# Kernel tuning notes

Measured on AMD Instinct MI355X. Metric: run time of the kernel, lower is better.

Reference implementation:

```python
import jax, jax.numpy as jnp
import numpy as np

B, S, E, H = 2, 2048, 1024, 16
D = E // H


def setup_inputs() -> dict:
    key = jax.random.key(0)
    ks = jax.random.split(key, 11)
    def lin(k):
        kw, kb = jax.random.split(k)
        bound = 1.0 / np.sqrt(E)
        W = jax.random.uniform(kw, (E, E), jnp.float32, -bound, bound)
        b = jax.random.uniform(kb, (E,), jnp.float32, -bound, bound)
        return W, b
    Wq, bq = lin(ks[0])
    Wk, bk = lin(ks[1])
    Wv, bv = lin(ks[2])
    Wo, bo = lin(ks[3])
    return {
        "query": jax.random.normal(ks[4], (B, S, E), jnp.float32),
        "key": jax.random.normal(ks[5], (B, S, E), jnp.float32),
        "value": jax.random.normal(ks[6], (B, S, E), jnp.float32),
        "Wq": Wq, "bq": bq, "Wk": Wk, "bk": bk,
        "Wv": Wv, "bv": bv, "Wo": Wo, "bo": bo,
        "is_causal": 1,
    }


def reference(query, key, value, Wq, bq, Wk, bk, Wv, bv, Wo, bo, is_causal):
    scale = D ** -0.5
    def heads(x, W, b):
        # torch Linear: x @ W.T + b, then [B,S,H,D] -> [B,H,S,D]
        y = jnp.einsum('bse,fe->bsf', x, W) + b
        return y.reshape(B, S, H, D).transpose(0, 2, 1, 3)
    q = heads(query, Wq, bq)
    k = heads(key, Wk, bk)
    v = heads(value, Wv, bv)
    scores = jnp.einsum('bhqd,bhkd->bhqk', q, k) * scale  # [B,H,S,S]
    if is_causal:
        mask = jnp.tril(jnp.ones((S, S), dtype=bool))
        scores = jnp.where(mask, scores, -jnp.inf)
    attn = jax.nn.softmax(scores, axis=-1)
    out = jnp.einsum('bhqk,bhkd->bhqd', attn, v)
    out = out.transpose(0, 2, 1, 3).reshape(B, S, E)
    return jnp.einsum('bse,fe->bsf', out, Wo) + bo
```

## Files before the change

kernel.cpp:

```cpp
#include <hip/hip_runtime.h>
#include <cstdint>
#include <cstddef>

typedef unsigned short u16;
typedef unsigned int u32;
typedef __attribute__((ext_vector_type(8))) short bf16x8;
typedef __attribute__((ext_vector_type(4))) float f32x4;
typedef __attribute__((ext_vector_type(16))) float f32x16;
typedef __attribute__((ext_vector_type(4))) u16 u16x4;
typedef __attribute__((ext_vector_type(4))) u32 u32x4;
typedef __attribute__((ext_vector_type(2))) u32 u32x2;

__device__ __forceinline__ u16 f2bf(float f) {
  u32 x = __builtin_bit_cast(u32, f);
  x += 0x7fffu + ((x >> 16) & 1u);
  return (u16)(x >> 16);
}

__device__ __forceinline__ void g2lds16(const u16* g, u16* l) {
  __builtin_amdgcn_global_load_lds(
      (const __attribute__((address_space(1))) u32*)g,
      (__attribute__((address_space(3))) u32*)l, 16, 0, 0);
}

struct CvtArgs { const float* s[7]; u16* d[7]; int n4[7]; };

__global__ __launch_bounds__(256) void cvt_all(CvtArgs a) {
  int y = blockIdx.y;
  const float4* __restrict__ src = (const float4*)a.s[y];
  u16* __restrict__ dst = a.d[y];
  int n4 = a.n4[y];
  for (int i = blockIdx.x * blockDim.x + threadIdx.x; i < n4;
       i += gridDim.x * blockDim.x) {
    float4 v = src[i];
    u16x4 o = { f2bf(v.x), f2bf(v.y), f2bf(v.z), f2bf(v.w) };
    *(u16x4*)(dst + (size_t)i * 4) = o;
  }
}

struct GemmArgs {
  const u16* A[3]; const u16* W[3]; const float* bias[3];
  void* out[3]; float scale[3]; int mode[3];
};

__global__ __launch_bounds__(256) void gemm_fused(GemmArgs ga) {
  __shared__ alignas(16) u16 As[2][128 * 32];
  __shared__ alignas(16) u16 Bs[2][128 * 32];
  const int z = blockIdx.z;
  const u16* __restrict__ A = ga.A[z];
  const u16* __restrict__ W = ga.W[z];
  const int tid = threadIdx.x;
  const int lane = tid & 63;
  const int w = tid >> 6;
  const int lo4 = lane & 15, hi2 = lane >> 4;
  const int l = (int)blockIdx.x + 8 * (int)blockIdx.y;
  const int wl = (l & 7) * 32 + (l >> 3);
  const int m0 = (wl >> 3) * 128;
  const int n0 = (wl & 7) * 128;
  const int wr = w >> 1, wc = w & 1;

  f32x4 acc[4][4] = {};

  auto stage = [&](int kt, int buf) {
    const int k0 = kt * 32;
#pragma unroll
    for (int i = 0; i < 2; ++i) {
      int c = (i * 4 + w) * 64 + lane;
      int r = c >> 2;
      int q = (c & 3) ^ ((r >> 1) & 3);
      g2lds16(A + (size_t)(m0 + r) * 1024 + k0 + q * 8, As[buf] + (i * 4 + w) * 512);
      g2lds16(W + (size_t)(n0 + r) * 1024 + k0 + q * 8, Bs[buf] + (i * 4 + w) * 512);
    }
  };

  stage(0, 0);
  __syncthreads();
  int cur = 0;
  for (int kt = 0; kt < 32; ++kt) {
    if (kt + 1 < 32) stage(kt + 1, cur ^ 1);
    bf16x8 af[4], bfr[4];
#pragma unroll
    for (int i = 0; i < 4; ++i) {
      int r = wr * 64 + i * 16 + lo4;
      int q = hi2 ^ ((r >> 1) & 3);
      af[i] = *(const bf16x8*)(As[cur] + r * 32 + q * 8);
    }
#pragma unroll
    for (int j = 0; j < 4; ++j) {
      int r = wc * 64 + j * 16 + lo4;
      int q = hi2 ^ ((r >> 1) & 3);
      bfr[j] = *(const bf16x8*)(Bs[cur] + r * 32 + q * 8);
    }
#pragma unroll
    for (int i = 0; i < 4; ++i)
#pragma unroll
      for (int j = 0; j < 4; ++j)
        acc[i][j] = __builtin_amdgcn_mfma_f32_16x16x32_bf16(af[i], bfr[j], acc[i][j], 0, 0, 0);
    __syncthreads();
    cur ^= 1;
  }

  const float* __restrict__ bias = ga.bias[z];
  const float cs = ga.scale[z];
  const int mode = ga.mode[z];
#pragma unroll
  for (int j = 0; j < 4; ++j) {
    int n = n0 + wc * 64 + j * 16 + lo4;
    float bv = bias[n];
#pragma unroll
    for (int i = 0; i < 4; ++i) {
#pragma unroll
      for (int rg = 0; rg < 4; ++rg) {
        int m = m0 + wr * 64 + i * 16 + hi2 * 4 + rg;
        float v = (acc[i][j][rg] + bv) * cs;
        if (mode == 2) {
          ((float*)ga.out[z])[(size_t)m * 1024 + n] = v;
        } else {
          int b = m >> 11, s = m & 2047, h = n >> 6, d = n & 63;
          size_t addr = (mode == 0)
            ? ((size_t)(b * 16 + h) * 2048 + s) * 64 + d
            : ((size_t)(b * 16 + h) * 64 + d) * 2048 + s;
          ((u16*)ga.out[z])[addr] = f2bf(v);
        }
      }
    }
  }
}

__global__ __launch_bounds__(256, 2) void attn_kernel(
    const u16* __restrict__ Q, const u16* __restrict__ K,
    const u16* __restrict__ Vt, u16* __restrict__ Out,
    const int* __restrict__ causal_p) {
  __shared__ alignas(16) u16 Ks[2][2][64 * 64];
  __shared__ alignas(16) u16 Vs[2][2][64 * 64];
  const int tid = threadIdx.x, lane = tid & 63, w = tid >> 6;
  const int wg = w >> 1, wv = w & 1;
  const int ql = lane & 31, hi = lane >> 5;
  const int bh = blockIdx.y;
  const int qt = (bh < 16) ? (int)blockIdx.x : 15 - (int)blockIdx.x;
  const int causal = *causal_p;
  const u16* Qb = Q + (size_t)bh * 2048 * 64;
  const u16* Kb = K + (size_t)bh * 2048 * 64;
  const u16* Vb = Vt + (size_t)bh * 64 * 2048;

  const int qA = qt * 128 + wv * 64 + ql;
  const int qB = qA + 32;

  bf16x8 qfA[4], qfB[4];
#pragma unroll
  for (int dsl = 0; dsl < 4; ++dsl) {
    qfA[dsl] = *(const bf16x8*)(Qb + (size_t)qA * 64 + dsl * 16 + hi * 8);
    qfB[dsl] = *(const bf16x8*)(Qb + (size_t)qB * 64 + dsl * 16 + hi * 8);
  }

  auto stageKV = [&](int jt, int buf) {
#pragma unroll
    for (int i = 0; i < 4; ++i) {
      int c = i * 128 + wv * 64 + lane;
      int r = c >> 3;
      int q = (c & 7) ^ (r & 7);
      g2lds16(Kb + (size_t)(jt * 64 + r) * 64 + q * 8, Ks[wg][buf] + (i * 128 + wv * 64) * 8);
      g2lds16(Vb + (size_t)r * 2048 + jt * 64 + q * 8, Vs[wg][buf] + (i * 128 + wv * 64) * 8);
    }
  };

  const int nt_w = causal ? (2 * qt + wv + 1) : 32;
  const int U = causal ? (qt + 1) : 16;

  stageKV(wg, 0);
  __syncthreads();

  float mA = -1e30f, lA = 0.f, mB = -1e30f, lB = 0.f;
  f32x16 oA0 = {}, oA1 = {}, oB0 = {}, oB1 = {};
  int cur = 0;

  auto online_sm = [&](f32x16& s0, f32x16& s1, float& m_r, float& l_r,
                       f32x16& o0, f32x16& o1) {
    float pm = fmaxf(s0[0], s1[0]);
#pragma unroll
    for (int rg = 1; rg < 16; ++rg) pm = fmaxf(pm, fmaxf(s0[rg], s1[rg]));
    pm = fmaxf(pm, __shfl_xor(pm, 32));
    if (!__all(pm <= m_r + 8.f)) {
      float mn = fmaxf(m_r, pm);
      float corr = exp2f(m_r - mn);
      m_r = mn; l_r *= corr;
#pragma unroll
      for (int rg = 0; rg < 16; ++rg) { o0[rg] *= corr; o1[rg] *= corr; }
    }
    float sum = 0.f;
#pragma unroll
    for (int rg = 0; rg < 16; ++rg) { s0[rg] = exp2f(s0[rg] - m_r); sum += s0[rg]; }
#pragma unroll
    for (int rg = 0; rg < 16; ++rg) { s1[rg] = exp2f(s1[rg] - m_r); sum += s1[rg]; }
    sum += __shfl_xor(sum, 32);
    l_r += sum;
  };

  for (int u = 0; u < U; ++u) {
    const int jt = 2 * u + wg;
    if (u + 1 < U) stageKV(jt + 2, cur ^ 1);

    if (jt < nt_w) {
      f32x16 sA0 = {}, sA1 = {}, sB0 = {}, sB1 = {};
#pragma unroll
      for (int dsl = 0; dsl < 4; ++dsl) {
        int cc = dsl * 2 + hi;
        bf16x8 k0 = *(const bf16x8*)(Ks[wg][cur] + ql * 64 + ((cc ^ (ql & 7)) * 8));
        bf16x8 k1 = *(const bf16x8*)(Ks[wg][cur] + (32 + ql) * 64 + ((cc ^ (ql & 7)) * 8));
        sA0 = __builtin_amdgcn_mfma_f32_32x32x16_bf16(k0, qfA[dsl], sA0, 0, 0, 0);
        sB0 = __builtin_amdgcn_mfma_f32_32x32x16_bf16(k0, qfB[dsl], sB0, 0, 0, 0);
        sA1 = __builtin_amdgcn_mfma_f32_32x32x16_bf16(k1, qfA[dsl], sA1, 0, 0, 0);
        sB1 = __builtin_amdgcn_mfma_f32_32x32x16_bf16(k1, qfB[dsl], sB1, 0, 0, 0);
      }

      if (causal && jt == nt_w - 1) {
#pragma unroll
        for (int rg = 0; rg < 16; ++rg) {
          int kof = jt * 64 + 8 * (rg >> 2) + (rg & 3) + 4 * hi;
          sA0[rg] = (kof > qA) ? -1e30f : sA0[rg];
          sA1[rg] = (kof + 32 > qA) ? -1e30f : sA1[rg];
          sB0[rg] = (kof > qB) ? -1e30f : sB0[rg];
          sB1[rg] = (kof + 32 > qB) ? -1e30f : sB1[rg];
        }
      }

      online_sm(sA0, sA1, mA, lA, oA0, oA1);
      online_sm(sB0, sB1, mB, lB, oB0, oB1);

#pragma unroll
      for (int s = 0; s < 4; ++s) {
        const f32x16& pA = (s >= 2) ? sA1 : sA0;
        const f32x16& pB = (s >= 2) ? sB1 : sB0;
        const int base = 8 * (s & 1);
        u32 a0, a1, b0, b1, c0, c1, d0_, d1;
        asm("v_cvt_pk_bf16_f32 %0, %1, %2" : "=v"(a0) : "v"(pA[base + 0]), "v"(pA[base + 1]));
        asm("v_cvt_pk_bf16_f32 %0, %1, %2" : "=v"(a1) : "v"(pA[base + 2]), "v"(pA[base + 3]));
        asm("v_cvt_pk_bf16_f32 %0, %1, %2" : "=v"(b0) : "v"(pA[base + 4]), "v"(pA[base + 5]));
        asm("v_cvt_pk_bf16_f32 %0, %1, %2" : "=v"(b1) : "v"(pA[base + 6]), "v"(pA[base + 7]));
        asm volatile("v_permlane32_swap_b32 %0, %1" : "+v"(a0), "+v"(b0));
        asm volatile("v_permlane32_swap_b32 %0, %1" : "+v"(a1), "+v"(b1));
        asm("v_cvt_pk_bf16_f32 %0, %1, %2" : "=v"(c0) : "v"(pB[base + 0]), "v"(pB[base + 1]));
        asm("v_cvt_pk_bf16_f32 %0, %1, %2" : "=v"(c1) : "v"(pB[base + 2]), "v"(pB[base + 3]));
        asm("v_cvt_pk_bf16_f32 %0, %1, %2" : "=v"(d0_) : "v"(pB[base + 4]), "v"(pB[base + 5]));
        asm("v_cvt_pk_bf16_f32 %0, %1, %2" : "=v"(d1) : "v"(pB[base + 6]), "v"(pB[base + 7]));
        asm volatile("v_permlane32_swap_b32 %0, %1" : "+v"(c0), "+v"(d0_));
        asm volatile("v_permlane32_swap_b32 %0, %1" : "+v"(c1), "+v"(d1));
        u32x4 pwA = {a0, a1, b0, b1};
        u32x4 pwB = {c0, c1, d0_, d1};
        bf16x8 pfA = __builtin_bit_cast(bf16x8, pwA);
        bf16x8 pfB = __builtin_bit_cast(bf16x8, pwB);
#pragma unroll
        for (int df = 0; df < 2; ++df) {
          int rr = df * 32 + ql;
          bf16x8 vf = *(const bf16x8*)(Vs[wg][cur] + rr * 64 + (((s * 2 + hi) ^ (rr & 7)) * 8));
          if (df) {
            oA1 = __builtin_amdgcn_mfma_f32_32x32x16_bf16(vf, pfA, oA1, 0, 0, 0);
            oB1 = __builtin_amdgcn_mfma_f32_32x32x16_bf16(vf, pfB, oB1, 0, 0, 0);
          } else {
            oA0 = __builtin_amdgcn_mfma_f32_32x32x16_bf16(vf, pfA, oA0, 0, 0, 0);
            oB0 = __builtin_amdgcn_mfma_f32_32x32x16_bf16(vf, pfB, oB0, 0, 0, 0);
          }
        }
      }
    }
    __syncthreads();
    cur ^= 1;
  }

  float* Od = (float*)&Ks[0][0][0];
  float* ml = (float*)&Vs[0][0][0];
  const int li = wv * 64 + lane;
  if (wg == 1) {
#pragma unroll
    for (int rg = 0; rg < 16; ++rg) {
      Od[((li * 2 + 0) * 2 + 0) * 16 + rg] = oA0[rg];
      Od[((li * 2 + 0) * 2 + 1) * 16 + rg] = oA1[rg];
      Od[((li * 2 + 1) * 2 + 0) * 16 + rg] = oB0[rg];
      Od[((li * 2 + 1) * 2 + 1) * 16 + rg] = oB1[rg];
    }
    ml[li * 4 + 0] = mA; ml[li * 4 + 1] = lA;
    ml[li * 4 + 2] = mB; ml[li * 4 + 3] = lB;
  }
  __syncthreads();
  if (wg == 0) {
    const int batch = bh >> 4, h = bh & 15;
#pragma unroll
    for (int sub = 0; sub < 2; ++sub) {
      float m_r = sub ? mB : mA;
      float l_r = sub ? lB : lA;
      float m_b = ml[li * 4 + sub * 2 + 0];
      float l_b = ml[li * 4 + sub * 2 + 1];
      float mn = fmaxf(m_r, m_b);
      float ca = exp2f(m_r - mn), cb = exp2f(m_b - mn);
      float rl = 1.f / (l_r * ca + l_b * cb);
      int qrow = sub ? qB : qA;
      u16* orow = Out + ((size_t)(batch * 2048 + qrow)) * 1024 + h * 64;
#pragma unroll
      for (int df = 0; df < 2; ++df) {
        const f32x16& oo = sub ? (df ? oB1 : oB0) : (df ? oA1 : oA0);
        const float* Op = &Od[((li * 2 + sub) * 2 + df) * 16];
#pragma unroll
        for (int b2 = 0; b2 < 4; ++b2) {
          u32 w0, w1;
          float v0 = (oo[4 * b2 + 0] * ca + Op[4 * b2 + 0] * cb) * rl;
          float v1 = (oo[4 * b2 + 1] * ca + Op[4 * b2 + 1] * cb) * rl;
          float v2 = (oo[4 * b2 + 2] * ca + Op[4 * b2 + 2] * cb) * rl;
          float v3 = (oo[4 * b2 + 3] * ca + Op[4 * b2 + 3] * cb) * rl;
          asm("v_cvt_pk_bf16_f32 %0, %1, %2" : "=v"(w0) : "v"(v0), "v"(v1));
          asm("v_cvt_pk_bf16_f32 %0, %1, %2" : "=v"(w1) : "v"(v2), "v"(v3));
          int d0 = df * 32 + b2 * 8 + hi * 4;
          u32x2 pr = {w0, w1};
          *(u32x2*)(orow + d0) = pr;
        }
      }
    }
  }
}

extern "C" void kernel_launch(void* const* d_in, const int* in_sizes, int n_in,
                              void* d_out, int out_size, void* d_ws, size_t ws_size,
                              hipStream_t stream) {
  (void)in_sizes; (void)n_in; (void)out_size; (void)ws_size;
  const float* query = (const float*)d_in[0];
  const float* key   = (const float*)d_in[1];
  const float* value = (const float*)d_in[2];
  const float* Wq = (const float*)d_in[3];
  const float* bq = (const float*)d_in[4];
  const float* Wk = (const float*)d_in[5];
  const float* bk = (const float*)d_in[6];
  const float* Wv = (const float*)d_in[7];
  const float* bv = (const float*)d_in[8];
  const float* Wo = (const float*)d_in[9];
  const float* bo = (const float*)d_in[10];
  const int* is_causal = (const int*)d_in[11];

  u16* wsp = (u16*)d_ws;
  u16* xq  = wsp;
  u16* xk  = xq  + (4u << 20);
  u16* xv  = xk  + (4u << 20);
  u16* wq  = xv  + (4u << 20);
  u16* wk  = wq  + (1u << 20);
  u16* wv  = wk  + (1u << 20);
  u16* wo  = wv  + (1u << 20);
  u16* Qb  = wo  + (1u << 20);
  u16* Kb  = Qb  + (4u << 20);
  u16* Vtb = Kb  + (4u << 20);
  u16* attn= Vtb + (4u << 20);

  CvtArgs ca;
  ca.s[0] = query; ca.d[0] = xq; ca.n4[0] = 1 << 20;
  ca.s[1] = key;   ca.d[1] = xk; ca.n4[1] = 1 << 20;
  ca.s[2] = value; ca.d[2] = xv; ca.n4[2] = 1 << 20;
  ca.s[3] = Wq; ca.d[3] = wq; ca.n4[3] = 1 << 18;
  ca.s[4] = Wk; ca.d[4] = wk; ca.n4[4] = 1 << 18;
  ca.s[5] = Wv; ca.d[5] = wv; ca.n4[5] = 1 << 18;
  ca.s[6] = Wo; ca.d[6] = wo; ca.n4[6] = 1 << 18;
  cvt_all<<<dim3(512, 7), 256, 0, stream>>>(ca);

  const float LOG2E = 1.4426950408889634f;
  GemmArgs g1;
  g1.A[0] = xq; g1.W[0] = wq; g1.bias[0] = bq; g1.out[0] = Qb;
  g1.scale[0] = 0.125f * LOG2E; g1.mode[0] = 0;
  g1.A[1] = xk; g1.W[1] = wk; g1.bias[1] = bk; g1.out[1] = Kb;
  g1.scale[1] = 1.f; g1.mode[1] = 0;
  g1.A[2] = xv; g1.W[2] = wv; g1.bias[2] = bv; g1.out[2] = Vtb;
  g1.scale[2] = 1.f; g1.mode[2] = 1;
  gemm_fused<<<dim3(8, 32, 3), 256, 0, stream>>>(g1);

  attn_kernel<<<dim3(16, 32), 256, 0, stream>>>(Qb, Kb, Vtb, attn, is_causal);

  GemmArgs g2;
  for (int i = 0; i < 3; ++i) {
    g2.A[i] = attn; g2.W[i] = wo; g2.bias[i] = bo; g2.out[i] = d_out;
    g2.scale[i] = 1.f; g2.mode[i] = 2;
  }
  gemm_fused<<<dim3(8, 32, 1), 256, 0, stream>>>(g2);
}
```

Measured before the change: 142.9 us.

## Replace GEMM with 256x256-tile 8-wave kernel using interleaved staging and MFMA priority

The projection GEMMs move from 128x128 tiles with 4 waves and K=32 steps to 256x256 tiles with 8 waves and K=64 steps. Global-to-LDS staging of the next k-tile is interleaved between four MFMA quadrants, with explicit vmcnt waits, barriers and setprio around the MFMA bursts. This is meant to raise arithmetic intensity and overlap memory with compute. The grid shrinks to 64 blocks per GEMM (192 for QKV), which may underfill the GPU, and the 128 KB of LDS per block limits occupancy.

New measurement: 170.2 us. 19.1% more time.

```diff
diff --git a/kernel.cpp b/kernel.cpp
--- a/kernel.cpp
+++ b/kernel.cpp
@@ -43,76 +43,123 @@
   void* out[3]; float scale[3]; int mode[3];
 };
 
-__global__ __launch_bounds__(256) void gemm_fused(GemmArgs ga) {
-  __shared__ alignas(16) u16 As[2][128 * 32];
-  __shared__ alignas(16) u16 Bs[2][128 * 32];
+__global__ __launch_bounds__(512, 2) void gemm8(GemmArgs ga) {
+  __shared__ alignas(16) u16 As[2][2][128 * 64];
+  __shared__ alignas(16) u16 Bs[2][2][128 * 64];
   const int z = blockIdx.z;
   const u16* __restrict__ A = ga.A[z];
   const u16* __restrict__ W = ga.W[z];
-  const int tid = threadIdx.x;
-  const int lane = tid & 63;
-  const int w = tid >> 6;
+  const int tid = threadIdx.x, lane = tid & 63, w = tid >> 6;
   const int lo4 = lane & 15, hi2 = lane >> 4;
-  const int l = (int)blockIdx.x + 8 * (int)blockIdx.y;
-  const int wl = (l & 7) * 32 + (l >> 3);
-  const int m0 = (wl >> 3) * 128;
-  const int n0 = (wl & 7) * 128;
-  const int wr = w >> 1, wc = w & 1;
-
-  f32x4 acc[4][4] = {};
-
-  auto stage = [&](int kt, int buf) {
-    const int k0 = kt * 32;
+  const int wr = w >> 2, wc = w & 3;
+  const int m0 = blockIdx.y * 256, n0 = blockIdx.x * 256;
+
+  f32x4 acc[8][4] = {};
+
+  auto stageA = [&](int kt, int hf) {
+    u16* lds = &As[kt & 1][hf][0];
+    const u16* src = A + (size_t)(m0 + hf * 128) * 1024 + (kt & 15) * 64;
 #pragma unroll
     for (int i = 0; i < 2; ++i) {
-      int c = (i * 4 + w) * 64 + lane;
-      int r = c >> 2;
-      int q = (c & 3) ^ ((r >> 1) & 3);
-      g2lds16(A + (size_t)(m0 + r) * 1024 + k0 + q * 8, As[buf] + (i * 4 + w) * 512);
-      g2lds16(W + (size_t)(n0 + r) * 1024 + k0 + q * 8, Bs[buf] + (i * 4 + w) * 512);
-    }
-  };
-
-  stage(0, 0);
-  __syncthreads();
-  int cur = 0;
-  for (int kt = 0; kt < 32; ++kt) {
-    if (kt + 1 < 32) stage(kt + 1, cur ^ 1);
-    bf16x8 af[4], bfr[4];
-#pragma unroll
-    for (int i = 0; i < 4; ++i) {
-      int r = wr * 64 + i * 16 + lo4;
-      int q = hi2 ^ ((r >> 1) & 3);
-      af[i] = *(const bf16x8*)(As[cur] + r * 32 + q * 8);
-    }
-#pragma unroll
-    for (int j = 0; j < 4; ++j) {
-      int r = wc * 64 + j * 16 + lo4;
-      int q = hi2 ^ ((r >> 1) & 3);
-      bfr[j] = *(const bf16x8*)(Bs[cur] + r * 32 + q * 8);
-    }
-#pragma unroll
-    for (int i = 0; i < 4; ++i)
-#pragma unroll
-      for (int j = 0; j < 4; ++j)
-        acc[i][j] = __builtin_amdgcn_mfma_f32_16x16x32_bf16(af[i], bfr[j], acc[i][j], 0, 0, 0);
-    __syncthreads();
-    cur ^= 1;
-  }
+      int c = i * 512 + tid;
+      int r = c >> 3;
+      int q = (c & 7) ^ (r & 7);
+      g2lds16(src + (size_t)r * 1024 + q * 8, lds + (i * 512 + w * 64) * 8);
+    }
+  };
+  auto stageB = [&](int kt, int hf) {
+    u16* lds = &Bs[kt & 1][hf][0];
+    const u16* src = W + (size_t)(n0 + hf * 128) * 1024 + (kt & 15) * 64;
+#pragma unroll
+    for (int i = 0; i < 2; ++i) {
+      int c = i * 512 + tid;
+      int r = c >> 3;
+      int q = (c & 7) ^ (r & 7);
+      g2lds16(src + (size_t)r * 1024 + q * 8, lds + (i * 512 + w * 64) * 8);
+    }
+  };
+
+  auto ldsA = [&](int buf, int gm, bf16x8 (*a)[2]) {
+#pragma unroll
+    for (int mi = 0; mi < 4; ++mi) {
+      int rh = gm * 64 + mi * 16 + lo4;
+#pragma unroll
+      for (int kk = 0; kk < 2; ++kk)
+        a[mi][kk] = *(const bf16x8*)(&As[buf][wr][0] + rh * 64 +
+                                     (((kk * 4 + hi2) ^ (rh & 7)) * 8));
+    }
+  };
+  auto ldsB = [&](int buf, int gn, bf16x8 (*b)[2]) {
+#pragma unroll
+    for (int nj = 0; nj < 2; ++nj) {
+      int rh = (wc & 1) * 64 + (gn * 2 + nj) * 16 + lo4;
+#pragma unroll
+      for (int kk = 0; kk < 2; ++kk)
+        b[nj][kk] = *(const bf16x8*)(&Bs[buf][wc >> 1][0] + rh * 64 +
+                                     (((kk * 4 + hi2) ^ (rh & 7)) * 8));
+    }
+  };
+  auto mfma16 = [&](int gm, int gn, bf16x8 (*a)[2], bf16x8 (*b)[2]) {
+#pragma unroll
+    for (int kk = 0; kk < 2; ++kk)
+#pragma unroll
+      for (int mi = 0; mi < 4; ++mi)
+#pragma unroll
+        for (int nj = 0; nj < 2; ++nj)
+          acc[gm * 4 + mi][gn * 2 + nj] = __builtin_amdgcn_mfma_f32_16x16x32_bf16(
+              a[mi][kk], b[nj][kk], acc[gm * 4 + mi][gn * 2 + nj], 0, 0, 0);
+  };
+
+  auto sync1 = [&]() {
+    __builtin_amdgcn_s_barrier();
+    asm volatile("s_waitcnt lgkmcnt(0)" ::: "memory");
+    __builtin_amdgcn_sched_barrier(0);
+    __builtin_amdgcn_s_setprio(1);
+  };
+  auto sync2 = [&]() {
+    __builtin_amdgcn_s_setprio(0);
+    __builtin_amdgcn_s_barrier();
+  };
+
+  stageB(0, 0); stageB(0, 1); stageA(0, 0); stageA(0, 1);
+  stageB(1, 0); stageB(1, 1); stageA(1, 0); stageA(1, 1);
+  asm volatile("s_waitcnt vmcnt(8)" ::: "memory");
+  __builtin_amdgcn_s_barrier();
+
+  auto ktile = [&](int buf, int ptile) {
+    bf16x8 a[4][2], b0[2][2], b1[2][2];
+    ldsA(buf, 0, a); ldsB(buf, 0, b0); ldsB(buf, 1, b1);
+    stageB(ptile, 0);
+    sync1(); mfma16(0, 0, a, b0); sync2();
+    stageB(ptile, 1);
+    sync1(); mfma16(0, 1, a, b1); sync2();
+    ldsA(buf, 1, a);
+    stageA(ptile, 0);
+    sync1(); mfma16(1, 1, a, b1); sync2();
+    stageA(ptile, 1);
+    asm volatile("s_waitcnt vmcnt(6)" ::: "memory");
+    sync1(); mfma16(1, 0, a, b0); sync2();
+  };
+
+  for (int it = 0; it < 8; ++it) {
+    ktile(0, (2 * it + 2) & 15);
+    ktile(1, (2 * it + 3) & 15);
+  }
+  asm volatile("s_waitcnt vmcnt(0)" ::: "memory");
 
   const float* __restrict__ bias = ga.bias[z];
   const float cs = ga.scale[z];
   const int mode = ga.mode[z];
 #pragma unroll
-  for (int j = 0; j < 4; ++j) {
-    int n = n0 + wc * 64 + j * 16 + lo4;
+  for (int j2 = 0; j2 < 4; ++j2) {
+    int n = n0 + wc * 64 + j2 * 16 + lo4;
     float bv = bias[n];
 #pragma unroll
-    for (int i = 0; i < 4; ++i) {
+    for (int i8 = 0; i8 < 8; ++i8) {
 #pragma unroll
       for (int rg = 0; rg < 4; ++rg) {
-        int m = m0 + wr * 64 + i * 16 + hi2 * 4 + rg;
-        float v = (acc[i][j][rg] + bv) * cs;
+        int m = m0 + wr * 128 + i8 * 16 + hi2 * 4 + rg;
+        float v = (acc[i8][j2][rg] + bv) * cs;
         if (mode == 2) {
           ((float*)ga.out[z])[(size_t)m * 1024 + n] = v;
         } else {
@@ -365,7 +412,7 @@
   g1.scale[1] = 1.f; g1.mode[1] = 0;
   g1.A[2] = xv; g1.W[2] = wv; g1.bias[2] = bv; g1.out[2] = Vtb;
   g1.scale[2] = 1.f; g1.mode[2] = 1;
-  gemm_fused<<<dim3(8, 32, 3), 256, 0, stream>>>(g1);
+  gemm8<<<dim3(4, 16, 3), 512, 0, stream>>>(g1);
 
   attn_kernel<<<dim3(16, 32), 256, 0, stream>>>(Qb, Kb, Vtb, attn, is_causal);
 
@@ -374,5 +421,5 @@
     g2.A[i] = attn; g2.W[i] = wo; g2.bias[i] = bo; g2.out[i] = d_out;
     g2.scale[i] = 1.f; g2.mode[i] = 2;
   }
-  gemm_fused<<<dim3(8, 32, 1), 256, 0, stream>>>(g2);
-}
+  gemm8<<<dim3(4, 16, 1), 512, 0, stream>>>(g2);
+}
```
